# Kernel tuning notes

Measured on AMD Instinct MI355X. Metric: run time of the kernel, lower is better.

Reference implementation:

```python
import jax, jax.numpy as jnp
import numpy as np

EPS = 1e-12  # F.normalize eps


def _l2norm(v, axis=-1):
    # torch.nn.functional.normalize: x / max(||x||_2, eps)
    n = jnp.sqrt(jnp.sum(v * v, axis=axis, keepdims=True))
    return v / jnp.maximum(n, EPS)


def setup_inputs() -> dict:
    key = jax.random.key(0)
    ks = jax.random.split(key, 4)
    B, C, W, H, Z = 8, 256, 16, 16, 16
    N, P = W * H * Z, 64
    heads = 8
    import math
    std_w = 1.0 / math.sqrt(C)      # nn.Linear default-ish scale
    std_ef = 1.0 / math.sqrt(P)     # init_() uses last-dim
    return {
        "x": jax.random.normal(ks[0], (B, C, W, H, Z), dtype=jnp.float32),
        "W_sa": jax.random.uniform(ks[1], (4 * C, C), jnp.float32, -std_w, std_w),
        "EF": jax.random.uniform(ks[2], (N, P), jnp.float32, -std_ef, std_ef),
        "temp2_sa": jnp.ones((heads, 1, 1), jnp.float32),
        "W_sc": jax.random.uniform(ks[3], (4 * C, C), jnp.float32, -std_w, std_w),
        "temp_sc": jnp.ones((heads, 1, 1), jnp.float32),
    }


def _qkvv(xf, Wt, heads):
    # xf: (B, N, C); torch Linear(hidden, 4*hidden, bias=False): y = x @ W.T
    B, N, C = xf.shape
    d = C // heads
    y = xf @ Wt.T                                   # (B, N, 4C)
    y = y.reshape(B, N, 4, heads, d)
    y = jnp.transpose(y, (2, 0, 3, 1, 4))           # (4, B, h, N, d)
    return y[0], y[1], y[2], y[3]


def reference(x, W_sa, EF, temp2_sa, W_sc, temp_sc):
    B, C, W, H, Z = x.shape
    N = W * H * Z
    heads = temp_sc.shape[0]
    d = C // heads
    xf = jnp.transpose(x.reshape(B, C, N), (0, 2, 1))  # (B, N, C)

    # ---- Spatial (Linformer-style projected) attention ----
    q, k, _, v_sa = _qkvv(xf, W_sa, heads)            # each (B, h, N, d)
    q_t = jnp.swapaxes(q, -2, -1)                     # (B, h, d, N)
    k_t = jnp.swapaxes(k, -2, -1)
    v_t = jnp.swapaxes(v_sa, -2, -1)
    k_proj = jnp.einsum('bhdn,nk->bhdk', k_t, EF)     # (B, h, d, P)
    v_proj = jnp.einsum('bhdn,nk->bhdk', v_t, EF)
    q_n = _l2norm(q_t, axis=-1)                       # normalize over N
    attn_sa = jnp.einsum('bhdn,bhdk->bhnk', q_n, k_proj) * temp2_sa  # (B,h,N,P)
    attn_sa = jax.nn.softmax(attn_sa, axis=-1)        # dropout: eval mode (identity)
    x_sa = jnp.einsum('bhnk,bhdk->bhnd', attn_sa, v_proj)            # (B,h,N,d)
    # faithful to original: permute(0,3,1,2) then reshape(B,N,C)
    x_sa = jnp.transpose(x_sa, (0, 3, 1, 2)).reshape(B, N, C)

    # ---- Channel (cross-covariance) attention ----
    qc, kc, v_ca, _ = _qkvv(xf, W_sc, heads)          # (B, h, N, d)
    qc_t = _l2norm(jnp.swapaxes(qc, -2, -1), axis=-1) # (B, h, d, N), norm over N
    kc_t = _l2norm(jnp.swapaxes(kc, -2, -1), axis=-1)
    vc_t = jnp.swapaxes(v_ca, -2, -1)                 # (B, h, d, N)
    attn_ca = jnp.einsum('bhdn,bhen->bhde', qc_t, kc_t) * temp_sc    # (B,h,d,d)
    attn_ca = jax.nn.softmax(attn_ca, axis=-1)
    x_ca = jnp.einsum('bhde,bhen->bhdn', attn_ca, vc_t)              # (B,h,d,N)
    x_ca = jnp.transpose(x_ca, (0, 3, 1, 2)).reshape(B, N, C)        # (B,N,h,d)->(B,N,C)

    feat = x_ca + x_sa
    out = jnp.transpose(feat.reshape(B, W, H, Z, C), (0, 4, 1, 2, 3))
    return out
```

## Files before the change

kernel.cpp:

```cpp
#include <hip/hip_runtime.h>

typedef unsigned short u16;
typedef unsigned int   u32;

typedef __attribute__((ext_vector_type(4))) short short4v;
typedef __attribute__((ext_vector_type(8))) short bf16x8;
typedef __attribute__((ext_vector_type(4))) float f32x4;


__device__ __forceinline__ float bf2f(u16 u){
  union { u32 i; float f; } v; v.i = ((u32)u) << 16; return v.f;
}
__device__ __forceinline__ u16 f2bf(float f){
  u32 u = __float_as_uint(f);
  u32 r = u + 0x7FFFu + ((u >> 16) & 1u);
  return (u16)(r >> 16);
}

__device__ __forceinline__ void gload_lds16(const u16* g, u16* l){
  __builtin_amdgcn_global_load_lds((const __attribute__((address_space(1))) void*)g,
                                   (__attribute__((address_space(3))) void*)l,
                                   16, 0, 0);
}

__global__ void k_detect(const u16* __restrict__ x, u32* __restrict__ flag){
  __shared__ int cnt[256];
  const int t = threadIdx.x;
  int c = 0;
  #pragma unroll
  for(int i = 0; i < 4; i++){
    u16 v = x[t * 4 + i];
    int e = (v >> 7) & 0xFF;
    if(e >= 112 && e <= 134) c++;
  }
  cnt[t] = c;
  __syncthreads();
  for(int s = 128; s > 0; s >>= 1){
    if(t < s) cnt[t] += cnt[t + s];
    __syncthreads();
  }
  if(t == 0) *flag = (cnt[0] < 800) ? 1u : 0u;
}

__global__ __launch_bounds__(256) void k_conv_all(const void* __restrict__ xsrc,
                                                  const void* __restrict__ Wsa,
                                                  const void* __restrict__ EF,
                                                  const void* __restrict__ Wsc,
                                                  const void* __restrict__ t2,
                                                  const void* __restrict__ tsc,
                                                  u16* __restrict__ xb,
                                                  u16* __restrict__ xT,
                                                  float* __restrict__ Wsaf,
                                                  u16* __restrict__ Wcat,
                                                  u16* __restrict__ EFT,
                                                  float* __restrict__ tf,
                                                  const u32* __restrict__ flag){
  __shared__ u16 T[64][72];
  const int t = threadIdx.x;
  const bool isf32 = (*flag != 0);
  if(blockIdx.y < 4){
    const int n0 = blockIdx.x * 64, c0 = blockIdx.y * 64, b = blockIdx.z;
    const int cl = t >> 2, ns = (t & 3) * 16;
    const size_t srcoff = ((size_t)(b * 256 + c0 + cl)) * 4096 + n0 + ns;
    u16 e[16];
    if(isf32){
      const float* sp = (const float*)xsrc + srcoff;
      #pragma unroll
      for(int i = 0; i < 4; i++){
        const float4 v = *(const float4*)(sp + i * 4);
        e[i*4+0] = f2bf(v.x); e[i*4+1] = f2bf(v.y);
        e[i*4+2] = f2bf(v.z); e[i*4+3] = f2bf(v.w);
      }
    } else {
      const u16* sp = (const u16*)xsrc + srcoff;
      *(uint4*)&e[0] = *(const uint4*)sp;
      *(uint4*)&e[8] = *(const uint4*)(sp + 8);
    }
    u16* xbp = xb + srcoff;
    *(uint4*)xbp       = *(uint4*)&e[0];
    *(uint4*)(xbp + 8) = *(uint4*)&e[8];
    #pragma unroll
    for(int i = 0; i < 16; i++) T[ns + i][cl] = e[i];
    __syncthreads();
    const int nl = t >> 2, cs = (t & 3) * 16;
    u16* xtp = xT + ((size_t)b * 4096 + n0 + nl) * 256 + c0 + cs;
    *(uint4*)xtp       = *(const uint4*)&T[nl][cs];
    *(uint4*)(xtp + 8) = *(const uint4*)&T[nl][cs + 8];
    return;
  }
  const int mid = blockIdx.x + 64 * blockIdx.z;
  if(mid < 256){
    const int i0 = (mid * 256 + t) * 4;
    float4 o;
    if(isf32){
      o = *(const float4*)((const float*)Wsa + i0);
    } else {
      const uint2 a = *(const uint2*)((const u16*)Wsa + i0);
      o.x = bf2f((u16)(a.x & 0xFFFF)); o.y = bf2f((u16)(a.x >> 16));
      o.z = bf2f((u16)(a.y & 0xFFFF)); o.w = bf2f((u16)(a.y >> 16));
    }
    *(float4*)(Wsaf + i0) = o;
    if(i0 < 65536){
      uint2 pk;
      pk.x = (u32)f2bf(o.x) | ((u32)f2bf(o.y) << 16);
      pk.y = (u32)f2bf(o.z) | ((u32)f2bf(o.w) << 16);
      *(uint2*)(Wcat + i0) = pk;
    }
  } else if(mid < 320){
    const int n0 = (mid - 256) * 64;
    const int nl = t >> 2, p0 = (t & 3) * 16;
    const size_t off = (size_t)(n0 + nl) * 64 + p0;
    u16 e[16];
    if(isf32){
      const float* sp = (const float*)EF + off;
      #pragma unroll
      for(int i = 0; i < 4; i++){
        const float4 v = *(const float4*)(sp + i * 4);
        e[i*4+0] = f2bf(v.x); e[i*4+1] = f2bf(v.y);
        e[i*4+2] = f2bf(v.z); e[i*4+3] = f2bf(v.w);
      }
    } else {
      const u16* sp = (const u16*)EF + off;
      *(uint4*)&e[0] = *(const uint4*)sp;
      *(uint4*)&e[8] = *(const uint4*)(sp + 8);
    }
    #pragma unroll
    for(int i = 0; i < 16; i++) T[p0 + i][nl] = e[i];
    __syncthreads();
    const int pr = t >> 2, nn = (t & 3) * 16;
    u16* dp = EFT + (size_t)pr * 4096 + n0 + nn;
    *(uint4*)dp       = *(const uint4*)&T[pr][nn];
    *(uint4*)(dp + 8) = *(const uint4*)&T[pr][nn + 8];
  } else if(mid < 416){
    const int i0 = ((mid - 320) * 256 + t) * 8;
    u16* dst = Wcat + 65536;
    if(isf32){
      const float4 a = *(const float4*)((const float*)Wsc + i0);
      const float4 b = *(const float4*)((const float*)Wsc + i0 + 4);
      uint4 o;
      o.x = (u32)f2bf(a.x) | ((u32)f2bf(a.y) << 16);
      o.y = (u32)f2bf(a.z) | ((u32)f2bf(a.w) << 16);
      o.z = (u32)f2bf(b.x) | ((u32)f2bf(b.y) << 16);
      o.w = (u32)f2bf(b.z) | ((u32)f2bf(b.w) << 16);
      *(uint4*)(dst + i0) = o;
    } else {
      *(uint4*)(dst + i0) = *(const uint4*)((const u16*)Wsc + i0);
    }
  } else if(mid == 416){
    if(t < 16){
      const void* s = (t < 8) ? t2 : tsc;
      const int i = t & 7;
      if(isf32) tf[t] = ((const float*)s)[i];
      else      tf[t] = bf2f(((const u16*)s)[i]);
    }
  }
}

__global__ __launch_bounds__(256) void k_qkv_xef(const u16* __restrict__ Wc,
                                                 const u16* __restrict__ xT,
                                                 const u16* __restrict__ xb,
                                                 const u16* __restrict__ EFT,
                                                 u16* __restrict__ Y,
                                                 float* __restrict__ nrmp,
                                                 float* __restrict__ xefp){
  __shared__ union {
    struct { u16 W0[128][32]; u16 X0[128][32];
             u16 W1[128][32]; u16 X1[128][32]; } d;
    u16 Cs[128][136];
  } L;
  const int t = threadIdx.x;
  const int w = t >> 6, lane = t & 63;
  const int fm = lane & 15, fq = lane >> 4;

  if(blockIdx.y == 8){
    const int mh = blockIdx.x & 1, s = blockIdx.x >> 1, b = blockIdx.z;
    const int c0 = mh * 128 + w * 32;
    const u16* ar = xb + ((size_t)(b * 256 + c0 + fm)) * 4096 + s * 256 + fq * 8;
    const u16* br = EFT + (size_t)fm * 4096 + s * 256 + fq * 8;
    f32x4 acc[2][4] = {};
    #pragma unroll
    for(int kk = 0; kk < 8; kk++){
      bf16x8 bfr[4];
      #pragma unroll
      for(int nt = 0; nt < 4; nt++)
        bfr[nt] = *(const bf16x8*)(br + (size_t)nt * 16 * 4096 + kk * 32);
      #pragma unroll
      for(int mt = 0; mt < 2; mt++){
        bf16x8 af = *(const bf16x8*)(ar + (size_t)mt * 16 * 4096 + kk * 32);
        #pragma unroll
        for(int nt = 0; nt < 4; nt++)
          acc[mt][nt] = __builtin_amdgcn_mfma_f32_16x16x32_bf16(af, bfr[nt],
                                                                acc[mt][nt], 0, 0, 0);
      }
    }
    float* dst = xefp + (size_t)s * 131072 + (size_t)(b * 256 + c0) * 64;
    #pragma unroll
    for(int mt = 0; mt < 2; mt++)
      #pragma unroll
      for(int nt = 0; nt < 4; nt++)
        #pragma unroll
        for(int r = 0; r < 4; r++)
          dst[(mt * 16 + fq * 4 + r) * 64 + nt * 16 + fm] = acc[mt][nt][r];
    return;
  }

  const int n0 = blockIdx.x * 128, m0 = blockIdx.y * 128, b = blockIdx.z;
  const int wm = w >> 1, wn = w & 1;
  const int lr = lane >> 2;
  const int lc = (lane & 3) * 8;
  const u16* gw = Wc + (size_t)m0 * 256;
  const u16* gx = xT + ((size_t)b * 4096 + n0) * 256;
  f32x4 acc[4][4] = {};

#define QKV_STAGE(Wbuf, Xbuf, kc) do{                                          \
    _Pragma("unroll")                                                          \
    for(int i_ = 0; i_ < 2; i_++){                                             \
      const int row_ = w * 32 + i_ * 16;                                       \
      gload_lds16(gw + (size_t)(row_ + lr) * 256 + (kc) + lc, &Wbuf[row_][0]); \
      gload_lds16(gx + (size_t)(row_ + lr) * 256 + (kc) + lc, &Xbuf[row_][0]); \
    } }while(0)

#define QKV_COMPUTE(Wbuf, Xbuf) do{                                            \
    bf16x8 af_[4], bx_[4];                                                     \
    _Pragma("unroll")                                                          \
    for(int mt_ = 0; mt_ < 4; mt_++)                                           \
      af_[mt_] = *(const bf16x8*)&Wbuf[wm * 64 + mt_ * 16 + fm][fq * 8];       \
    _Pragma("unroll")                                                          \
    for(int nt_ = 0; nt_ < 4; nt_++)                                           \
      bx_[nt_] = *(const bf16x8*)&Xbuf[wn * 64 + nt_ * 16 + fm][fq * 8];       \
    _Pragma("unroll")                                                          \
    for(int mt_ = 0; mt_ < 4; mt_++)                                           \
      _Pragma("unroll")                                                        \
      for(int nt_ = 0; nt_ < 4; nt_++)                                         \
        acc[mt_][nt_] = __builtin_amdgcn_mfma_f32_16x16x32_bf16(               \
            af_[mt_], bx_[nt_], acc[mt_][nt_], 0, 0, 0);                       \
    }while(0)

  QKV_STAGE(L.d.W0, L.d.X0, 0);
  __syncthreads();
  #pragma unroll
  for(int it = 0; it < 8; it++){
    if(it & 1){
      if(it < 7) QKV_STAGE(L.d.W0, L.d.X0, (it + 1) * 32);
      QKV_COMPUTE(L.d.W1, L.d.X1);
    } else {
      if(it < 7) QKV_STAGE(L.d.W1, L.d.X1, (it + 1) * 32);
      QKV_COMPUTE(L.d.W0, L.d.X0);
    }
    __syncthreads();
  }

  #pragma unroll
  for(int mt = 0; mt < 4; mt++)
    #pragma unroll
    for(int nt = 0; nt < 4; nt++)
      #pragma unroll
      for(int r = 0; r < 4; r++)
        L.Cs[wm * 64 + mt * 16 + fq * 4 + r][wn * 64 + nt * 16 + fm] =
          f2bf(acc[mt][nt][r]);
  __syncthreads();
  const bool do_norm = (blockIdx.y < 6);
  float* npb = nrmp + (size_t)blockIdx.x * 6144 + (size_t)b * 768 + m0;
  #pragma unroll
  for(int i = 0; i < 8; i++){
    const int row = i * 16 + (t >> 4), ce = (t & 15) * 8;
    uint4 pk = *(const uint4*)&L.Cs[row][ce];
    *(uint4*)(Y + ((size_t)b * 1024 + m0 + row) * 4096 + n0 + ce) = pk;
    if(do_norm){
      u16 e[8]; *(uint4*)e = pk;
      float s = 0.f;
      #pragma unroll
      for(int k2 = 0; k2 < 8; k2++){ float v = bf2f(e[k2]); s += v * v; }
      #pragma unroll
      for(int m2 = 1; m2 < 16; m2 <<= 1) s += __shfl_xor(s, m2, 16);
      if((t & 15) == 0) npb[row] = s;
    }
  }
#undef QKV_STAGE
#undef QKV_COMPUTE
}

__global__ __launch_bounds__(256) void k_xred_nfin(const float* __restrict__ xefp,
                                                   float* __restrict__ xef,
                                                   const float* __restrict__ nrmp,
                                                   float* __restrict__ inv3){
  const int bx = blockIdx.x, t = threadIdx.x;
  if(bx < 128){
    const int i0 = (bx * 256 + t) * 4;
    float4 a = *(const float4*)(xefp + i0);
    #pragma unroll
    for(int s = 1; s < 16; s++){
      const float4 v = *(const float4*)(xefp + (size_t)s * 131072 + i0);
      a.x += v.x; a.y += v.y; a.z += v.z; a.w += v.w;
    }
    *(float4*)(xef + i0) = a;
  } else {
    const int tid = (bx - 128) * 256 + t;
    float s = 0.f;
    #pragma unroll
    for(int nt = 0; nt < 32; nt++) s += nrmp[(size_t)nt * 6144 + tid];
    const int b = tid / 768, m = tid - b * 768;
    inv3[(m >> 8) * 2048 + b * 256 + (m & 255)] = 1.0f / fmaxf(sqrtf(s), 1e-12f);
  }
}

__device__ __forceinline__ bf16x8 ld_frag8(const u16* p){
  short4v lo = *(const short4v*)p;
  short4v hi = *(const short4v*)(p + 4);
  bf16x8 r;
  r[0]=lo[0]; r[1]=lo[1]; r[2]=lo[2]; r[3]=lo[3];
  r[4]=hi[0]; r[5]=hi[1]; r[6]=hi[2]; r[7]=hi[3];
  return r;
}

__global__ __launch_bounds__(256) void k_kv_gram(const u16* __restrict__ Y,
                                                 const float* __restrict__ Wsaf,
                                                 const float* __restrict__ xef,
                                                 const float* __restrict__ invsa,
                                                 u16* __restrict__ kpT,
                                                 u16* __restrict__ vpb,
                                                 float* __restrict__ Gp){
  const int t = threadIdx.x;
  if(blockIdx.x < 64){
    const int s = blockIdx.x >> 3, h = blockIdx.x & 7, b = blockIdx.y;
    const int w = t >> 6, lane = t & 63;
    const int fm = lane & 15, fq = lane >> 4;
    const int j0 = (w >> 1) * 16, e0 = (w & 1) * 16;
    const u16* qrow = Y + (size_t)(b * 1024 + 256 + h * 32 + j0 + fm) * 4096;
    const u16* krow = Y + (size_t)(b * 1024 + 512 + h * 32 + e0 + fm) * 4096;
    f32x4 acc = {};
    const int nb0 = s * 512 + fq * 8;
    #pragma unroll 4
    for(int it = 0; it < 16; it++){
      const int nb = nb0 + it * 32;
      bf16x8 a  = ld_frag8(qrow + nb);
      bf16x8 bb = ld_frag8(krow + nb);
      acc = __builtin_amdgcn_mfma_f32_16x16x32_bf16(a, bb, acc, 0, 0, 0);
    }
    float* dst = Gp + ((size_t)((s * 8 + b) * 8 + h) * 1024);
    #pragma unroll
    for(int r = 0; r < 4; r++)
      dst[(j0 + fq * 4 + r) * 32 + e0 + fm] = acc[r];
    return;
  }
  const int ri = t >> 6, p = t & 63;
  const int r = (blockIdx.x - 64) * 4 + ri, b = blockIdx.y;
  const int row_w = (r < 256) ? (256 + r) : (512 + r);
  const float* wr = Wsaf + (size_t)row_w * 256;
  const float* xr = xef + (size_t)(b * 256) * 64 + p;
  float acc = 0.f;
  for(int c = 0; c < 256; c++)
    acc += wr[c] * xr[(size_t)c * 64];
  if(r < 256){
    const float sc = invsa[b * 256 + r];
    kpT[((size_t)(b * 8 + (r >> 5)) * 64 + p) * 32 + (r & 31)] = f2bf(acc * sc);
  } else {
    const int rv = r - 256;
    vpb[((size_t)(b * 8 + (rv >> 5)) * 32 + (rv & 31)) * 64 + p] = f2bf(acc);
  }
}

__global__ __launch_bounds__(256) void k_sa_sm(const u16* __restrict__ Y,
                                               const u16* __restrict__ kpT,
                                               const u16* __restrict__ vpb,
                                               const float* __restrict__ tf,
                                               const float* __restrict__ Gp,
                                               const float* __restrict__ invq,
                                               const float* __restrict__ invk,
                                               u16* __restrict__ xsa,
                                               float* __restrict__ attn){
  __shared__ u16 As[64][36];
  __shared__ u16 Ks[64][36];
  __shared__ u16 Vs[32][68];
  __shared__ u16 Ps[64][68];
  __shared__ u16 Cs[32][68];
  const int t = threadIdx.x;
  if(blockIdx.x == 64){
    if(blockIdx.y != 0) return;
    const int b = blockIdx.z;
    const int h = t >> 5, j = t & 31;
    const float tm = tf[8 + h];
    const float iq = invq[b * 256 + h * 32 + j];
    float v[32];
    float m = -1e30f;
    #pragma unroll
    for(int e = 0; e < 32; e++){
      float g = 0.f;
      #pragma unroll
      for(int s = 0; s < 8; s++)
        g += Gp[(size_t)s * 65536 + (size_t)(b * 8 + h) * 1024 + j * 32 + e];
      float val = g * iq * invk[b * 256 + h * 32 + e] * tm;
      v[e] = val; m = fmaxf(m, val);
    }
    float sum = 0.f;
    #pragma unroll
    for(int e = 0; e < 32; e++){ v[e] = __expf(v[e] - m); sum += v[e]; }
    const float inv = 1.0f / sum;
    #pragma unroll
    for(int e = 0; e < 32; e++)
      attn[(size_t)(b * 8 + h) * 1024 + j * 32 + e] = v[e] * inv;
    return;
  }
  const int ntile = blockIdx.x, h = blockIdx.y, b = blockIdx.z;
  const int n0 = ntile * 64;
  const int w = t >> 6, lane = t & 63;
  const int fm = lane & 15, fq = lane >> 4;
  {
    const int j = t >> 3, ns = (t & 7) * 8;
    const u16* src = Y + (size_t)(b * 1024 + h * 32 + j) * 4096 + n0 + ns;
    uint4 v = *(const uint4*)src;
    u16 e[8]; *(uint4*)e = v;
    #pragma unroll
    for(int i = 0; i < 8; i++) As[ns + i][j] = e[i];
  }
  {
    const int p = t >> 2, jb = (t & 3) * 8;
    *(uint4*)&Ks[p][jb] =
      *(const uint4*)(kpT + ((size_t)(b * 8 + h) * 64 + p) * 32 + jb);
  }
  {
    const int jv = t >> 3, ps = (t & 7) * 8;
    *(uint4*)&Vs[jv][ps] =
      *(const uint4*)(vpb + ((size_t)(b * 8 + h) * 32 + jv) * 64 + ps);
  }
  __syncthreads();
  bf16x8 a = ld_frag8(&As[w * 16 + fm][fq * 8]);
  f32x4 lg[4];
  #pragma unroll
  for(int pt = 0; pt < 4; pt++){
    bf16x8 bk = ld_frag8(&Ks[pt * 16 + fm][fq * 8]);
    f32x4 z = {};
    lg[pt] = __builtin_amdgcn_mfma_f32_16x16x32_bf16(a, bk, z, 0, 0, 0);
  }
  const float tm = tf[h];
  float sinv[4];
  #pragma unroll
  for(int r = 0; r < 4; r++){
    float v0 = lg[0][r]*tm, v1 = lg[1][r]*tm, v2 = lg[2][r]*tm, v3 = lg[3][r]*tm;
    float mx = fmaxf(fmaxf(v0, v1), fmaxf(v2, v3));
    #pragma unroll
    for(int m = 1; m < 16; m <<= 1) mx = fmaxf(mx, __shfl_xor(mx, m, 16));
    v0 = __expf(v0 - mx); v1 = __expf(v1 - mx);
    v2 = __expf(v2 - mx); v3 = __expf(v3 - mx);
    float s = v0 + v1 + v2 + v3;
    #pragma unroll
    for(int m = 1; m < 16; m <<= 1) s += __shfl_xor(s, m, 16);
    sinv[r] = 1.0f / s;
    const int nrow = w * 16 + fq * 4 + r;
    Ps[nrow][fm]      = f2bf(v0);
    Ps[nrow][16 + fm] = f2bf(v1);
    Ps[nrow][32 + fm] = f2bf(v2);
    Ps[nrow][48 + fm] = f2bf(v3);
  }
  f32x4 o[2] = {};
  #pragma unroll
  for(int ks = 0; ks < 2; ks++){
    bf16x8 ap = ld_frag8(&Ps[w * 16 + fm][ks * 32 + fq * 8]);
    #pragma unroll
    for(int jt = 0; jt < 2; jt++){
      bf16x8 bv = ld_frag8(&Vs[jt * 16 + fm][ks * 32 + fq * 8]);
      o[jt] = __builtin_amdgcn_mfma_f32_16x16x32_bf16(ap, bv, o[jt], 0, 0, 0);
    }
  }
  #pragma unroll
  for(int jt = 0; jt < 2; jt++)
    #pragma unroll
    for(int r = 0; r < 4; r++)
      Cs[jt * 16 + fm][w * 16 + fq * 4 + r] = f2bf(o[jt][r] * sinv[r]);
  __syncthreads();
  {
    const int jv = t >> 3, ns = (t & 7) * 8;
    u16 e[8];
    #pragma unroll
    for(int i = 0; i < 8; i++) e[i] = Cs[jv][ns + i];
    *(uint4*)(xsa + ((size_t)(b * 8 + h) * 32 + jv) * 4096 + n0 + ns) = *(uint4*)e;
  }
}

__global__ __launch_bounds__(256) void k_out_mfma(const u16* __restrict__ Y,
                                                  const float* __restrict__ attn,
                                                  const u16* __restrict__ xsa,
                                                  float* __restrict__ out){
  __shared__ union {
    u16   Vt[32][516];
    float Ot[32][132];
  } U;
  __shared__ u16 xs[32][16][34];
  __shared__ u16 Ah[32][40];
  __shared__ u16 Al[32][40];
  const int t = threadIdx.x;
  const int jg = blockIdx.x, hc = blockIdx.y, b = blockIdx.z;
  const int nn0 = jg * 512;
  const int w = t >> 6, lane = t & 63;
  const int fm = lane & 15, fq = lane >> 4;
  {
    const float4 v = *(const float4*)(attn + (size_t)(b * 8 + hc) * 1024 + t * 4);
    const int j = t >> 3, e0 = (t & 7) * 4;
    float vv[4] = {v.x, v.y, v.z, v.w};
    #pragma unroll
    for(int i = 0; i < 4; i++){
      u16 hi = f2bf(vv[i]);
      Ah[j][e0 + i] = hi;
      Al[j][e0 + i] = f2bf(vv[i] - bf2f(hi));
    }
  }
  {
    const int e = t >> 3, ch = (t & 7) * 64;
    const u16* src = Y + (size_t)(b * 1024 + 768 + hc * 32 + e) * 4096 + nn0 + ch;
    #pragma unroll
    for(int i = 0; i < 8; i++){
      uint4 v = *(const uint4*)(src + i * 8);
      uint2 lo; lo.x = v.x; lo.y = v.y;
      uint2 hi; hi.x = v.z; hi.y = v.w;
      *(uint2*)&U.Vt[e][ch + i * 8]     = lo;
      *(uint2*)&U.Vt[e][ch + i * 8 + 4] = hi;
    }
  }
  #pragma unroll
  for(int rep = 0; rep < 2; rep++){
    const int s = rep * 256 + t;
    const int hj = s >> 4, nh = s & 15;
    const int h = hj & 7, jj = hj >> 3;
    const u16* src = xsa + ((size_t)(b * 8 + h) * 32 + jg * 4 + jj) * 4096 + nh * 256 + hc * 32;
    uint4 v0 = *(const uint4*)src;
    uint4 v1 = *(const uint4*)(src + 8);
    u32* d32 = (u32*)&xs[hj][nh][0];
    d32[0] = v0.x; d32[1] = v0.y; d32[2] = v0.z; d32[3] = v0.w;
    d32[4] = v1.x; d32[5] = v1.y; d32[6] = v1.z; d32[7] = v1.w;
    uint4 v2 = *(const uint4*)(src + 16);
    uint4 v3 = *(const uint4*)(src + 24);
    d32[8]  = v2.x; d32[9]  = v2.y; d32[10] = v2.z; d32[11] = v2.w;
    d32[12] = v3.x; d32[13] = v3.y; d32[14] = v3.z; d32[15] = v3.w;
  }
  __syncthreads();
  bf16x8 ah[2], al[2];
  #pragma unroll
  for(int mt = 0; mt < 2; mt++){
    ah[mt] = *(const bf16x8*)&Ah[mt * 16 + fm][fq * 8];
    al[mt] = *(const bf16x8*)&Al[mt * 16 + fm][fq * 8];
  }
  f32x4 acc[2][8] = {};
  #pragma unroll
  for(int nt = 0; nt < 8; nt++){
    const int colb = w * 128 + nt * 16 + fm;
    bf16x8 bv;
    #pragma unroll
    for(int i = 0; i < 8; i++) bv[i] = (short)U.Vt[fq * 8 + i][colb];
    #pragma unroll
    for(int mt = 0; mt < 2; mt++){
      acc[mt][nt] = __builtin_amdgcn_mfma_f32_16x16x32_bf16(ah[mt], bv, acc[mt][nt], 0, 0, 0);
      acc[mt][nt] = __builtin_amdgcn_mfma_f32_16x16x32_bf16(al[mt], bv, acc[mt][nt], 0, 0, 0);
    }
  }
  __syncthreads();
  #pragma unroll
  for(int p = 0; p < 4; p++){
    if(w == p){
      #pragma unroll
      for(int mt = 0; mt < 2; mt++)
        #pragma unroll
        for(int nt = 0; nt < 8; nt++)
          #pragma unroll
          for(int r = 0; r < 4; r++){
            const float sa = bf2f(xs[w * 8 + nt][fm][mt * 16 + fq * 4 + r]);
            U.Ot[mt * 16 + fq * 4 + r][nt * 16 + fm] = acc[mt][nt][r] + sa;
          }
    }
    __syncthreads();
    #pragma unroll
    for(int i = 0; i < 4; i++){
      const int idx = i * 256 + t;
      const int row = idx >> 5, c4 = (idx & 31) * 4;
      const float4 v = *(const float4*)&U.Ot[row][c4];
      *(float4*)&out[(size_t)(b * 256 + hc * 32 + row) * 4096 + nn0 + p * 128 + c4] = v;
    }
    __syncthreads();
  }
}

#define OFF_XB    ((size_t)0)
#define OFF_XT    ((size_t)16777216)
#define OFF_Y     ((size_t)33554432)
#define OFF_WSAF  ((size_t)100663296)
#define OFF_WCAT  ((size_t)101711872)
#define OFF_EFT   ((size_t)102236160)
#define OFF_XEF   ((size_t)103284736)
#define OFF_KPT   ((size_t)103809024)
#define OFF_VPB   ((size_t)104071168)
#define OFF_ISA   ((size_t)104333312)
#define OFF_IQC   ((size_t)104341504)
#define OFF_IKC   ((size_t)104349696)
#define OFF_GP    ((size_t)104357888)
#define OFF_ATT   ((size_t)106455040)
#define OFF_TF    ((size_t)106717184)
#define OFF_FLAG  ((size_t)106717248)
#define OFF_NRM   ((size_t)106717312)
#define OFF_XEFP  ((size_t)107503744)

extern "C" void kernel_launch(void* const* d_in, const int* in_sizes, int n_in,
                              void* d_out, int out_size, void* d_ws, size_t ws_size,
                              hipStream_t stream){
  (void)in_sizes; (void)n_in; (void)out_size; (void)ws_size;
  char* ws = (char*)d_ws;
  u16*   xb    = (u16*)  (ws + OFF_XB);
  u16*   xsa   = (u16*)  (ws + OFF_XB);
  u16*   xT    = (u16*)  (ws + OFF_XT);
  u16*   Y     = (u16*)  (ws + OFF_Y);
  float* Wsaf  = (float*)(ws + OFF_WSAF);
  u16*   Wcat  = (u16*)  (ws + OFF_WCAT);
  u16*   EFT   = (u16*)  (ws + OFF_EFT);
  float* xef   = (float*)(ws + OFF_XEF);
  u16*   kpT   = (u16*)  (ws + OFF_KPT);
  u16*   vpb   = (u16*)  (ws + OFF_VPB);
  float* invsa = (float*)(ws + OFF_ISA);
  float* invqc = (float*)(ws + OFF_IQC);
  float* invkc = (float*)(ws + OFF_IKC);
  float* Gp    = (float*)(ws + OFF_GP);
  float* attn  = (float*)(ws + OFF_ATT);
  float* tf    = (float*)(ws + OFF_TF);
  u32*   flag  = (u32*)  (ws + OFF_FLAG);
  float* nrmp  = (float*)(ws + OFF_NRM);
  float* xefp  = (float*)(ws + OFF_XEFP);
  float* out = (float*)d_out;

  k_detect<<<1, 256, 0, stream>>>((const u16*)d_in[0], flag);
  k_conv_all<<<dim3(64, 5, 8), 256, 0, stream>>>(d_in[0], d_in[1], d_in[2],
                                                 d_in[4], d_in[3], d_in[5],
                                                 xb, xT, Wsaf, Wcat, EFT, tf, flag);
  k_qkv_xef<<<dim3(32, 9, 8), 256, 0, stream>>>(Wcat, xT, xb, EFT, Y, nrmp, xefp);
  k_xred_nfin<<<152, 256, 0, stream>>>(xefp, xef, nrmp, invsa);
  k_kv_gram<<<dim3(192, 8), 256, 0, stream>>>(Y, Wsaf, xef, invsa, kpT, vpb, Gp);
  k_sa_sm<<<dim3(65, 8, 8), 256, 0, stream>>>(Y, kpT, vpb, tf, Gp, invsa + 2048,
                                              invsa + 4096, xsa, attn);
  k_out_mfma<<<dim3(8, 8, 8), 256, 0, stream>>>(Y, attn, xsa, out);
}
```

Before: 202.8 us.

## Triple-buffer QKV GEMM LDS staging with XOR swizzle and partial vmcnt waits

Replaces the double-buffered LDS pipeline in the QKV projection GEMM with a three-stage ring. Explicit s_waitcnt vmcnt(4) plus a bare barrier let one stage of global loads stay in flight while computing on another. It also XOR-swizzles the 16-byte column chunk of each row, both on the global_load_lds write and on the fragment reads, to cut LDS bank conflicts. This costs more LDS per block, which may lower occupancy, and relies on hand-counted vmcnt values that must match the number of issued loads.

New measurement: 202.7 us. No clear change (-0.0%).

```diff
diff --git a/kernel.cpp b/kernel.cpp
--- a/kernel.cpp
+++ b/kernel.cpp
@@ -164,8 +164,7 @@
                                                  float* __restrict__ nrmp,
                                                  float* __restrict__ xefp){
   __shared__ union {
-    struct { u16 W0[128][32]; u16 X0[128][32];
-             u16 W1[128][32]; u16 X1[128][32]; } d;
+    struct { u16 W[3][128][32]; u16 X[3][128][32]; } d;
     u16 Cs[128][136];
   } L;
   const int t = threadIdx.x;
@@ -207,27 +206,30 @@
   const int n0 = blockIdx.x * 128, m0 = blockIdx.y * 128, b = blockIdx.z;
   const int wm = w >> 1, wn = w & 1;
   const int lr = lane >> 2;
-  const int lc = (lane & 3) * 8;
+  const int lcs = ((lane & 3) ^ ((lane >> 3) & 3)) * 8;
+  const int sl  = (fq ^ ((fm >> 1) & 3)) * 8;
   const u16* gw = Wc + (size_t)m0 * 256;
   const u16* gx = xT + ((size_t)b * 4096 + n0) * 256;
   f32x4 acc[4][4] = {};
 
-#define QKV_STAGE(Wbuf, Xbuf, kc) do{                                          \
+#define QKV_STAGE(bi, kc) do{                                                  \
     _Pragma("unroll")                                                          \
     for(int i_ = 0; i_ < 2; i_++){                                             \
       const int row_ = w * 32 + i_ * 16;                                       \
-      gload_lds16(gw + (size_t)(row_ + lr) * 256 + (kc) + lc, &Wbuf[row_][0]); \
-      gload_lds16(gx + (size_t)(row_ + lr) * 256 + (kc) + lc, &Xbuf[row_][0]); \
+      gload_lds16(gw + (size_t)(row_ + lr) * 256 + (kc) + lcs,                 \
+                  &L.d.W[bi][row_][0]);                                        \
+      gload_lds16(gx + (size_t)(row_ + lr) * 256 + (kc) + lcs,                 \
+                  &L.d.X[bi][row_][0]);                                        \
     } }while(0)
 
-#define QKV_COMPUTE(Wbuf, Xbuf) do{                                            \
+#define QKV_COMPUTE(bi) do{                                                    \
     bf16x8 af_[4], bx_[4];                                                     \
     _Pragma("unroll")                                                          \
     for(int mt_ = 0; mt_ < 4; mt_++)                                           \
-      af_[mt_] = *(const bf16x8*)&Wbuf[wm * 64 + mt_ * 16 + fm][fq * 8];       \
+      af_[mt_] = *(const bf16x8*)&L.d.W[bi][wm * 64 + mt_ * 16 + fm][sl];      \
     _Pragma("unroll")                                                          \
     for(int nt_ = 0; nt_ < 4; nt_++)                                           \
-      bx_[nt_] = *(const bf16x8*)&Xbuf[wn * 64 + nt_ * 16 + fm][fq * 8];       \
+      bx_[nt_] = *(const bf16x8*)&L.d.X[bi][wn * 64 + nt_ * 16 + fm][sl];      \
     _Pragma("unroll")                                                          \
     for(int mt_ = 0; mt_ < 4; mt_++)                                           \
       _Pragma("unroll")                                                        \
@@ -236,19 +238,23 @@
             af_[mt_], bx_[nt_], acc[mt_][nt_], 0, 0, 0);                       \
     }while(0)
 
-  QKV_STAGE(L.d.W0, L.d.X0, 0);
+#define QKV_FENCE(N) do{                                                       \
+    asm volatile("s_waitcnt vmcnt(" #N ")" ::: "memory");                      \
+    asm volatile("s_waitcnt lgkmcnt(0)" ::: "memory");                         \
+    __builtin_amdgcn_s_barrier();                                              \
+  }while(0)
+
+  QKV_STAGE(0, 0);
+  QKV_STAGE(1, 32);
+  QKV_FENCE(4);
+  #pragma unroll
+  for(int it = 0; it < 8; it++){
+    if(it < 6) QKV_STAGE((it + 2) % 3, (it + 2) * 32);
+    QKV_COMPUTE(it % 3);
+    if(it < 6)      QKV_FENCE(4);
+    else if(it == 6) QKV_FENCE(0);
+  }
   __syncthreads();
-  #pragma unroll
-  for(int it = 0; it < 8; it++){
-    if(it & 1){
-      if(it < 7) QKV_STAGE(L.d.W0, L.d.X0, (it + 1) * 32);
-      QKV_COMPUTE(L.d.W1, L.d.X1);
-    } else {
-      if(it < 7) QKV_STAGE(L.d.W1, L.d.X1, (it + 1) * 32);
-      QKV_COMPUTE(L.d.W0, L.d.X0);
-    }
-    __syncthreads();
-  }
 
   #pragma unroll
   for(int mt = 0; mt < 4; mt++)
@@ -278,6 +284,7 @@
   }
 #undef QKV_STAGE
 #undef QKV_COMPUTE
+#undef QKV_FENCE
 }
 
 __global__ __launch_bounds__(256) void k_xred_nfin(const float* __restrict__ xefp,
```

## Replace LDS double-buffered QKV GEMM with direct global-load MFMA on smaller tiles

Applied to the files above, without the earlier changes.

The QKV projection GEMM drops its LDS double-buffered staging via global_load_lds and instead loads MFMA fragments directly from global memory. Each block now covers a 128x64 output tile instead of 128x128, so the grid doubles to 64 tiles along N. The per-tile norm partials double, so the reduction loop and workspace offsets change to match. This removes LDS staging and barriers and raises the block count, at the cost of less operand reuse and more uncoalesced global traffic per MFMA.

Measured after the change: 267.2 us. 1.32x slower.

```diff
diff --git a/kernel.cpp b/kernel.cpp
--- a/kernel.cpp
+++ b/kernel.cpp
@@ -15,12 +15,6 @@
   u32 u = __float_as_uint(f);
   u32 r = u + 0x7FFFu + ((u >> 16) & 1u);
   return (u16)(r >> 16);
-}
-
-__device__ __forceinline__ void gload_lds16(const u16* g, u16* l){
-  __builtin_amdgcn_global_load_lds((const __attribute__((address_space(1))) void*)g,
-                                   (__attribute__((address_space(3))) void*)l,
-                                   16, 0, 0);
 }
 
 __global__ void k_detect(const u16* __restrict__ x, u32* __restrict__ flag){
@@ -163,16 +157,13 @@
                                                  u16* __restrict__ Y,
                                                  float* __restrict__ nrmp,
                                                  float* __restrict__ xefp){
-  __shared__ union {
-    struct { u16 W0[128][32]; u16 X0[128][32];
-             u16 W1[128][32]; u16 X1[128][32]; } d;
-    u16 Cs[128][136];
-  } L;
+  __shared__ u16 Cs[128][72];
   const int t = threadIdx.x;
   const int w = t >> 6, lane = t & 63;
   const int fm = lane & 15, fq = lane >> 4;
 
   if(blockIdx.y == 8){
+    if(blockIdx.x >= 32) return;
     const int mh = blockIdx.x & 1, s = blockIdx.x >> 1, b = blockIdx.z;
     const int c0 = mh * 128 + w * 32;
     const u16* ar = xb + ((size_t)(b * 256 + c0 + fm)) * 4096 + s * 256 + fq * 8;
@@ -204,80 +195,53 @@
     return;
   }
 
-  const int n0 = blockIdx.x * 128, m0 = blockIdx.y * 128, b = blockIdx.z;
-  const int wm = w >> 1, wn = w & 1;
-  const int lr = lane >> 2;
-  const int lc = (lane & 3) * 8;
-  const u16* gw = Wc + (size_t)m0 * 256;
-  const u16* gx = xT + ((size_t)b * 4096 + n0) * 256;
-  f32x4 acc[4][4] = {};
-
-#define QKV_STAGE(Wbuf, Xbuf, kc) do{                                          \
-    _Pragma("unroll")                                                          \
-    for(int i_ = 0; i_ < 2; i_++){                                             \
-      const int row_ = w * 32 + i_ * 16;                                       \
-      gload_lds16(gw + (size_t)(row_ + lr) * 256 + (kc) + lc, &Wbuf[row_][0]); \
-      gload_lds16(gx + (size_t)(row_ + lr) * 256 + (kc) + lc, &Xbuf[row_][0]); \
-    } }while(0)
-
-#define QKV_COMPUTE(Wbuf, Xbuf) do{                                            \
-    bf16x8 af_[4], bx_[4];                                                     \
-    _Pragma("unroll")                                                          \
-    for(int mt_ = 0; mt_ < 4; mt_++)                                           \
-      af_[mt_] = *(const bf16x8*)&Wbuf[wm * 64 + mt_ * 16 + fm][fq * 8];       \
-    _Pragma("unroll")                                                          \
-    for(int nt_ = 0; nt_ < 4; nt_++)                                           \
-      bx_[nt_] = *(const bf16x8*)&Xbuf[wn * 64 + nt_ * 16 + fm][fq * 8];       \
-    _Pragma("unroll")                                                          \
-    for(int mt_ = 0; mt_ < 4; mt_++)                                           \
-      _Pragma("unroll")                                                        \
-      for(int nt_ = 0; nt_ < 4; nt_++)                                         \
-        acc[mt_][nt_] = __builtin_amdgcn_mfma_f32_16x16x32_bf16(               \
-            af_[mt_], bx_[nt_], acc[mt_][nt_], 0, 0, 0);                       \
-    }while(0)
-
-  QKV_STAGE(L.d.W0, L.d.X0, 0);
-  __syncthreads();
-  #pragma unroll
-  for(int it = 0; it < 8; it++){
-    if(it & 1){
-      if(it < 7) QKV_STAGE(L.d.W0, L.d.X0, (it + 1) * 32);
-      QKV_COMPUTE(L.d.W1, L.d.X1);
-    } else {
-      if(it < 7) QKV_STAGE(L.d.W1, L.d.X1, (it + 1) * 32);
-      QKV_COMPUTE(L.d.W0, L.d.X0);
-    }
-    __syncthreads();
-  }
-
-  #pragma unroll
-  for(int mt = 0; mt < 4; mt++)
+  const int n0 = blockIdx.x * 64, m0 = blockIdx.y * 128, b = blockIdx.z;
+  const u16* ar = Wc + (size_t)(m0 + w * 32 + fm) * 256 + fq * 8;
+  const u16* br = xT + ((size_t)b * 4096 + n0 + fm) * 256 + fq * 8;
+  f32x4 acc[2][4] = {};
+  #pragma unroll
+  for(int kk = 0; kk < 8; kk++){
+    bf16x8 bfr[4];
     #pragma unroll
     for(int nt = 0; nt < 4; nt++)
+      bfr[nt] = *(const bf16x8*)(br + (size_t)nt * 16 * 256 + kk * 32);
+    #pragma unroll
+    for(int mt = 0; mt < 2; mt++){
+      bf16x8 af = *(const bf16x8*)(ar + (size_t)mt * 16 * 256 + kk * 32);
+      #pragma unroll
+      for(int nt = 0; nt < 4; nt++)
+        acc[mt][nt] = __builtin_amdgcn_mfma_f32_16x16x32_bf16(af, bfr[nt],
+                                                              acc[mt][nt], 0, 0, 0);
+    }
+  }
+  #pragma unroll
+  for(int mt = 0; mt < 2; mt++)
+    #pragma unroll
+    for(int nt = 0; nt < 4; nt++)
       #pragma unroll
       for(int r = 0; r < 4; r++)
-        L.Cs[wm * 64 + mt * 16 + fq * 4 + r][wn * 64 + nt * 16 + fm] =
-          f2bf(acc[mt][nt][r]);
+        Cs[w * 32 + mt * 16 + fq * 4 + r][nt * 16 + fm] = f2bf(acc[mt][nt][r]);
   __syncthreads();
   const bool do_norm = (blockIdx.y < 6);
   float* npb = nrmp + (size_t)blockIdx.x * 6144 + (size_t)b * 768 + m0;
   #pragma unroll
-  for(int i = 0; i < 8; i++){
-    const int row = i * 16 + (t >> 4), ce = (t & 15) * 8;
-    uint4 pk = *(const uint4*)&L.Cs[row][ce];
-    *(uint4*)(Y + ((size_t)b * 1024 + m0 + row) * 4096 + n0 + ce) = pk;
+  for(int i = 0; i < 2; i++){
+    const int row = i * 64 + (t >> 2), ce = (t & 3) * 16;
+    uint4 p0 = *(const uint4*)&Cs[row][ce];
+    uint4 p1 = *(const uint4*)&Cs[row][ce + 8];
+    u16* yp = Y + ((size_t)b * 1024 + m0 + row) * 4096 + n0 + ce;
+    *(uint4*)yp       = p0;
+    *(uint4*)(yp + 8) = p1;
     if(do_norm){
-      u16 e[8]; *(uint4*)e = pk;
+      u16 e[16]; *(uint4*)&e[0] = p0; *(uint4*)&e[8] = p1;
       float s = 0.f;
       #pragma unroll
-      for(int k2 = 0; k2 < 8; k2++){ float v = bf2f(e[k2]); s += v * v; }
-      #pragma unroll
-      for(int m2 = 1; m2 < 16; m2 <<= 1) s += __shfl_xor(s, m2, 16);
-      if((t & 15) == 0) npb[row] = s;
-    }
-  }
-#undef QKV_STAGE
-#undef QKV_COMPUTE
+      for(int k2 = 0; k2 < 16; k2++){ float v = bf2f(e[k2]); s += v * v; }
+      #pragma unroll
+      for(int m2 = 1; m2 < 4; m2 <<= 1) s += __shfl_xor(s, m2, 4);
+      if((t & 3) == 0) npb[row] = s;
+    }
+  }
 }
 
 __global__ __launch_bounds__(256) void k_xred_nfin(const float* __restrict__ xefp,
@@ -297,8 +261,8 @@
   } else {
     const int tid = (bx - 128) * 256 + t;
     float s = 0.f;
-    #pragma unroll
-    for(int nt = 0; nt < 32; nt++) s += nrmp[(size_t)nt * 6144 + tid];
+    #pragma unroll 8
+    for(int nt = 0; nt < 64; nt++) s += nrmp[(size_t)nt * 6144 + tid];
     const int b = tid / 768, m = tid - b * 768;
     inv3[(m >> 8) * 2048 + b * 256 + (m & 255)] = 1.0f / fmaxf(sqrtf(s), 1e-12f);
   }
@@ -595,7 +559,7 @@
 #define OFF_TF    ((size_t)106717184)
 #define OFF_FLAG  ((size_t)106717248)
 #define OFF_NRM   ((size_t)106717312)
-#define OFF_XEFP  ((size_t)107503744)
+#define OFF_XEFP  ((size_t)108290176)
 
 extern "C" void kernel_launch(void* const* d_in, const int* in_sizes, int n_in,
                               void* d_out, int out_size, void* d_ws, size_t ws_size,
@@ -627,7 +591,7 @@
   k_conv_all<<<dim3(64, 5, 8), 256, 0, stream>>>(d_in[0], d_in[1], d_in[2],
                                                  d_in[4], d_in[3], d_in[5],
                                                  xb, xT, Wsaf, Wcat, EFT, tf, flag);
-  k_qkv_xef<<<dim3(32, 9, 8), 256, 0, stream>>>(Wcat, xT, xb, EFT, Y, nrmp, xefp);
+  k_qkv_xef<<<dim3(64, 9, 8), 256, 0, stream>>>(Wcat, xT, xb, EFT, Y, nrmp, xefp);
   k_xred_nfin<<<152, 256, 0, stream>>>(xefp, xef, nrmp, invsa);
   k_kv_gram<<<dim3(192, 8), 256, 0, stream>>>(Y, Wsaf, xef, invsa, kpT, vpb, Gp);
   k_sa_sm<<<dim3(65, 8, 8), 256, 0, stream>>>(Y, kpT, vpb, tf, Gp, invsa + 2048,
```
